# Optimization experiments

Hardware: AMD Instinct MI355X
Metric: run time of the kernel (lower is better)

Reference implementation:

```python
import jax, jax.numpy as jnp
import numpy as np

TEMPERATURE = 11.313708498984761  # sqrt(128)


def setup_inputs() -> dict:
    key = jax.random.key(0)
    kq, kk, kv = jax.random.split(key, 3)
    b, n, m, d, dv = 16, 2048, 2048, 128, 128
    return {
        "queries": jax.random.normal(kq, (b, n, d), dtype=jnp.float32),
        "keys": jax.random.normal(kk, (b, m, d), dtype=jnp.float32),
        "values": jax.random.normal(kv, (b, m, dv), dtype=jnp.float32),
    }


def reference(queries, keys, values):
    # scores: [b, n, m]
    scores = jnp.einsum('bnd,bmd->bnm', queries, keys) / TEMPERATURE
    attn = jax.nn.softmax(scores, axis=2)
    # out: [b, n, d']
    return jnp.einsum('bnm,bmd->bnd', attn, values)
```

## Files before the change

### kernel.cpp

```cpp
#include <hip/hip_runtime.h>


#define BATCH 16
#define SEQ   2048
#define DIM   128
#define NT    (SEQ / 64)

typedef short bf16x8 __attribute__((ext_vector_type(8)));
typedef float f32x16 __attribute__((ext_vector_type(16)));

static __device__ __forceinline__ unsigned pk2(float lo, float hi) {
  union { float f; unsigned u; } a, b;
  a.f = lo; b.f = hi;
  return ((b.u + 0x8000u) & 0xffff0000u) | ((a.u + 0x8000u) >> 16);
}
static __device__ __forceinline__ float fast_exp2(float x) {
#if __has_builtin(__builtin_amdgcn_exp2f)
  return __builtin_amdgcn_exp2f(x);
#else
  return exp2f(x);
#endif
}

typedef __attribute__((address_space(1))) const unsigned int g_u32;
typedef __attribute__((address_space(3))) unsigned int l_u32;
static __device__ __forceinline__ void gl2lds16(const unsigned short* g, unsigned short* l) {
  __builtin_amdgcn_global_load_lds((g_u32*)g, (l_u32*)l, 16, 0, 0);
}

__global__ __launch_bounds__(256)
void prep_kernel(const float* __restrict__ K, const float* __restrict__ V,
                 unsigned short* __restrict__ Kb, unsigned short* __restrict__ Vt,
                 float scale) {
  const int bx = blockIdx.x, tid = threadIdx.x;
  if (bx < 2048) {
    size_t idx = (size_t)bx * 256 + tid;
    const float4* kf = (const float4*)K;
    float4 a = kf[idx * 2], c = kf[idx * 2 + 1];
    uint4 o;
    o.x = pk2(a.x * scale, a.y * scale);
    o.y = pk2(a.z * scale, a.w * scale);
    o.z = pk2(c.x * scale, c.y * scale);
    o.w = pk2(c.z * scale, c.w * scale);
    ((uint4*)Kb)[idx] = o;
  } else {
    __shared__ float tile[128][33];
    const int vb = bx - 2048;
    const int b = vb >> 6, r = vb & 63;
    const int m0 = (r & 15) * 128, d0 = (r >> 4) * 32;
    const int c = tid & 7, mr = tid >> 3;
    const float* src = V + ((size_t)(b * SEQ) + m0) * DIM + d0;
#pragma unroll
    for (int it = 0; it < 4; ++it) {
      int m = it * 32 + mr;
      float4 x = *(const float4*)(src + (size_t)m * DIM + c * 4);
      tile[m][c * 4 + 0] = x.x; tile[m][c * 4 + 1] = x.y;
      tile[m][c * 4 + 2] = x.z; tile[m][c * 4 + 3] = x.w;
    }
    __syncthreads();
    const int dr = tid >> 3, s = tid & 7;
    unsigned short* dst = Vt + ((size_t)(b * DIM) + d0 + dr) * SEQ + m0;
#pragma unroll
    for (int it = 0; it < 2; ++it) {
      int slot = it * 8 + s;
      uint4 o;
      o.x = pk2(tile[slot * 8 + 0][dr], tile[slot * 8 + 1][dr]);
      o.y = pk2(tile[slot * 8 + 2][dr], tile[slot * 8 + 3][dr]);
      o.z = pk2(tile[slot * 8 + 4][dr], tile[slot * 8 + 5][dr]);
      o.w = pk2(tile[slot * 8 + 6][dr], tile[slot * 8 + 7][dr]);
      *(uint4*)(dst + slot * 8) = o;
    }
  }
}


__global__ __launch_bounds__(256, 2)
void attn_kernel(const float* __restrict__ Qf,
                 const unsigned short* __restrict__ Kb,
                 const unsigned short* __restrict__ Vtb,
                 float* __restrict__ out) {
  __shared__ __align__(1024) unsigned char smem[65536];
  unsigned short* sm16 = (unsigned short*)smem;

  const int tid  = threadIdx.x;
  const int wv   = tid >> 6;
  const int w_q  = wv & 1;
  const int w_m  = wv >> 1;
  const int lane = tid & 63;
  const int l31  = lane & 31;
  const int q2   = lane >> 5;
  const int b    = blockIdx.x;
  const int q0   = blockIdx.y * 64 + w_q * 32;

  const unsigned short* kb = Kb  + (size_t)b * SEQ * DIM;
  const unsigned short* vb = Vtb + (size_t)b * SEQ * DIM;

  bf16x8 aq[8];
  {
    const float* qp = Qf + ((size_t)(b * SEQ) + q0 + l31) * DIM + q2 * 8;
#pragma unroll
    for (int c = 0; c < 8; ++c) {
      float4 x = *(const float4*)(qp + c * 16);
      float4 y = *(const float4*)(qp + c * 16 + 4);
      union { unsigned i[4]; bf16x8 v; } u;
      u.i[0] = pk2(x.x, x.y); u.i[1] = pk2(x.z, x.w);
      u.i[2] = pk2(y.x, y.y); u.i[3] = pk2(y.z, y.w);
      aq[c] = u.v;
    }
  }

  unsigned kgo[4], vgo[4];
#pragma unroll
  for (int i = 0; i < 4; ++i) {
    int ch = wv * 4 + i;
    int krow = ch * 4 + (lane >> 4);
    kgo[i] = (unsigned)(krow * 128) + ((((lane & 15) << 4) ^ ((krow & 15) << 4)) >> 1);
    int vrow = ch * 8 + (lane >> 3);
    vgo[i] = (unsigned)(vrow * 2048) + ((((lane & 7) << 4) ^ ((vrow & 7) << 4)) >> 1);
  }

  const int kro = ((w_m * 32 + l31) << 8) + ((q2 << 4) ^ ((l31 & 15) << 4));
  const int vro = (l31 << 7) + (((w_m << 6) + (q2 << 4)) ^ ((l31 & 7) << 4));

  f32x16 oacc[4];
#pragma unroll
  for (int t = 0; t < 4; ++t)
#pragma unroll
    for (int i = 0; i < 16; ++i) oacc[t][i] = 0.0f;
  float lsum = 0.0f;

#define STAGE(TK, BUF) do {                                                  \
    const unsigned short* kt_b = kb + ((size_t)(TK) << 13);                  \
    const unsigned short* vt_b = vb + ((TK) << 6);                           \
    unsigned short* kd = sm16 + (((BUF) + wv * 4096) >> 1);                  \
    unsigned short* vd = sm16 + ((32768 + (BUF) + wv * 4096) >> 1);          \
    _Pragma("unroll")                                                        \
    for (int i = 0; i < 4; ++i) gl2lds16(kt_b + kgo[i], kd + i * 512);       \
    _Pragma("unroll")                                                        \
    for (int i = 0; i < 4; ++i) gl2lds16(vt_b + vgo[i], vd + i * 512);       \
  } while (0)

  STAGE(0, 0);

  for (int kt = 0; kt < NT; ++kt) {
    const int cur = (kt & 1) << 14;
    __syncthreads();
    if (kt + 1 < NT) STAGE(kt + 1, 16384 - cur);

    const unsigned char* kB = smem + cur;
    const unsigned char* vB = smem + 32768 + cur;

    f32x16 s;
#pragma unroll
    for (int i = 0; i < 16; ++i) s[i] = 0.0f;
    __builtin_amdgcn_s_setprio(1);
#pragma unroll
    for (int c = 0; c < 8; ++c) {
      bf16x8 bk = *(const bf16x8*)(kB + (kro ^ (c << 5)));
      s = __builtin_amdgcn_mfma_f32_32x32x16_bf16(bk, aq[c], s, 0, 0, 0);
    }
    __builtin_amdgcn_s_setprio(0);

    float p[16];
#pragma unroll
    for (int i = 0; i < 16; ++i) { p[i] = fast_exp2(s[i]); lsum += p[i]; }

    unsigned d0 = pk2(p[0], p[1]),   d1 = pk2(p[2], p[3]);
    unsigned d2 = pk2(p[4], p[5]),   d3 = pk2(p[6], p[7]);
    unsigned d4 = pk2(p[8], p[9]),   d5 = pk2(p[10], p[11]);
    unsigned d6 = pk2(p[12], p[13]), d7 = pk2(p[14], p[15]);
    asm("v_permlane32_swap_b32 %0, %1" : "+v"(d0), "+v"(d2));
    asm("v_permlane32_swap_b32 %0, %1" : "+v"(d1), "+v"(d3));
    asm("v_permlane32_swap_b32 %0, %1" : "+v"(d4), "+v"(d6));
    asm("v_permlane32_swap_b32 %0, %1" : "+v"(d5), "+v"(d7));
    union { unsigned u[4]; bf16x8 v; } pu0, pu1;
    pu0.u[0] = d0; pu0.u[1] = d1; pu0.u[2] = d2; pu0.u[3] = d3;
    pu1.u[0] = d4; pu1.u[1] = d5; pu1.u[2] = d6; pu1.u[3] = d7;

    __builtin_amdgcn_s_setprio(1);
#pragma unroll
    for (int t = 0; t < 4; ++t) {
      bf16x8 bv0 = *(const bf16x8*)(vB + t * 4096 + vro);
      oacc[t] = __builtin_amdgcn_mfma_f32_32x32x16_bf16(pu0.v, bv0, oacc[t], 0, 0, 0);
      bf16x8 bv1 = *(const bf16x8*)(vB + t * 4096 + (vro ^ 32));
      oacc[t] = __builtin_amdgcn_mfma_f32_32x32x16_bf16(pu1.v, bv1, oacc[t], 0, 0, 0);
    }
    __builtin_amdgcn_s_setprio(0);
  }
#undef STAGE

  lsum += __shfl_xor(lsum, 32, 64);

  __syncthreads();
  float* cb  = (float*)smem;
  float* cbL = (float*)(smem + 32768);
  if (w_m == 1) {
    float* my = cb + w_q * 4096;
#pragma unroll
    for (int t = 0; t < 4; ++t)
#pragma unroll
      for (int r = 0; r < 16; ++r)
        my[(t * 16 + r) * 64 + lane] = oacc[t][r];
  }
  cbL[w_m * 64 + w_q * 32 + l31] = lsum;
  __syncthreads();
  if (w_m == 0) {
    const float* pr = cb + w_q * 4096;
    float linv[16];
#pragma unroll
    for (int r = 0; r < 16; ++r) {
      int qr = (r & 3) + ((r >> 2) << 3) + (q2 << 2);
      linv[r] = 1.0f / (cbL[w_q * 32 + qr] + cbL[64 + w_q * 32 + qr]);
    }
    float* ob = out + ((size_t)(b * SEQ) + q0) * DIM;
#pragma unroll
    for (int t = 0; t < 4; ++t)
#pragma unroll
      for (int r = 0; r < 16; ++r) {
        int qr = (r & 3) + ((r >> 2) << 3) + (q2 << 2);
        ob[(size_t)qr * DIM + t * 32 + l31] = (oacc[t][r] + pr[(t * 16 + r) * 64 + lane]) * linv[r];
      }
  }
}

extern "C" void kernel_launch(void* const* d_in, const int* in_sizes, int n_in,
                              void* d_out, int out_size, void* d_ws, size_t ws_size,
                              hipStream_t stream) {
  const float* Q = (const float*)d_in[0];
  const float* K = (const float*)d_in[1];
  const float* V = (const float*)d_in[2];
  float* out = (float*)d_out;

  const size_t elems = (size_t)BATCH * SEQ * DIM;
  unsigned short* Kb = (unsigned short*)d_ws;
  unsigned short* Vt = Kb + elems;

  const double TEMPERATURE = 11.313708498984761;
  const float scale = (float)(1.4426950408889634 / TEMPERATURE);

  prep_kernel<<<3072, 256, 0, stream>>>(K, V, Kb, Vt, scale);
  attn_kernel<<<dim3(BATCH, SEQ / 64), 256, 0, stream>>>(Q, Kb, Vt, out);
}
```

Measured before the change: 136.5 us.

## Software-pipeline QK of next tile with softmax and PV of current tile

Restructures the attention loop into a two-stage software pipeline, so the QK^T MFMAs for tile k+1 are issued before the exp/convert/PV work for tile k. V fragments are preloaded into registers before the barrier, letting the stage buffer be reused earlier. The QK chain is split into two independent accumulators, row sums use four partial accumulators, and the manual bf16 rounding is replaced by the hardware v_cvt_pk_bf16_f32 instruction. This shortens dependency chains and overlaps the matrix units with the vector units, at the cost of higher register pressure and possible occupancy loss.

```diff
diff --git a/kernel.cpp b/kernel.cpp
--- a/kernel.cpp
+++ b/kernel.cpp
@@ -127,7 +127,7 @@
   for (int t = 0; t < 4; ++t)
 #pragma unroll
     for (int i = 0; i < 16; ++i) oacc[t][i] = 0.0f;
-  float lsum = 0.0f;
+  float ls[4] = {0.0f, 0.0f, 0.0f, 0.0f};
 
 #define STAGE(TK, BUF) do {                                                  \
     const unsigned short* kt_b = kb + ((size_t)(TK) << 13);                  \
@@ -140,55 +140,120 @@
     for (int i = 0; i < 4; ++i) gl2lds16(vt_b + vgo[i], vd + i * 512);       \
   } while (0)
 
+#define VLOAD(CUR) do {                                                      \
+    const unsigned char* vB_ = smem + 32768 + (CUR);                         \
+    _Pragma("unroll")                                                        \
+    for (int t = 0; t < 4; ++t) {                                            \
+      vr[2 * t]     = *(const bf16x8*)(vB_ + t * 4096 + vro);                \
+      vr[2 * t + 1] = *(const bf16x8*)(vB_ + t * 4096 + (vro ^ 32));         \
+    }                                                                        \
+  } while (0)
+
+#define QK(CUR, SD) do {                                                     \
+    const unsigned char* kB_ = smem + (CUR);                                 \
+    f32x16 se, so;                                                           \
+    _Pragma("unroll")                                                        \
+    for (int i = 0; i < 16; ++i) { se[i] = 0.0f; so[i] = 0.0f; }             \
+    __builtin_amdgcn_s_setprio(1);                                           \
+    _Pragma("unroll")                                                        \
+    for (int c = 0; c < 4; ++c) {                                            \
+      bf16x8 b0 = *(const bf16x8*)(kB_ + (kro ^ ((2 * c) << 5)));            \
+      se = __builtin_amdgcn_mfma_f32_32x32x16_bf16(b0, aq[2 * c], se, 0, 0, 0); \
+      bf16x8 b1 = *(const bf16x8*)(kB_ + (kro ^ ((2 * c + 1) << 5)));        \
+      so = __builtin_amdgcn_mfma_f32_32x32x16_bf16(b1, aq[2 * c + 1], so, 0, 0, 0); \
+    }                                                                        \
+    __builtin_amdgcn_s_setprio(0);                                           \
+    _Pragma("unroll")                                                        \
+    for (int i = 0; i < 16; ++i) SD[i] = se[i] + so[i];                      \
+  } while (0)
+
+#define SOFTMAX(S, PU0, PU1) do {                                            \
+    float p[16];                                                             \
+    _Pragma("unroll")                                                        \
+    for (int i = 0; i < 16; ++i) p[i] = fast_exp2(S[i]);                     \
+    _Pragma("unroll")                                                        \
+    for (int i = 0; i < 4; ++i) {                                            \
+      ls[0] += p[4 * i + 0]; ls[1] += p[4 * i + 1];                          \
+      ls[2] += p[4 * i + 2]; ls[3] += p[4 * i + 3];                          \
+    }                                                                        \
+    unsigned d0, d1, d2, d3, d4, d5, d6, d7;                                 \
+    asm("v_cvt_pk_bf16_f32 %0, %1, %2" : "=v"(d0) : "v"(p[0]),  "v"(p[1]));  \
+    asm("v_cvt_pk_bf16_f32 %0, %1, %2" : "=v"(d1) : "v"(p[2]),  "v"(p[3]));  \
+    asm("v_cvt_pk_bf16_f32 %0, %1, %2" : "=v"(d2) : "v"(p[4]),  "v"(p[5]));  \
+    asm("v_cvt_pk_bf16_f32 %0, %1, %2" : "=v"(d3) : "v"(p[6]),  "v"(p[7]));  \
+    asm("v_cvt_pk_bf16_f32 %0, %1, %2" : "=v"(d4) : "v"(p[8]),  "v"(p[9]));  \
+    asm("v_cvt_pk_bf16_f32 %0, %1, %2" : "=v"(d5) : "v"(p[10]), "v"(p[11])); \
+    asm("v_cvt_pk_bf16_f32 %0, %1, %2" : "=v"(d6) : "v"(p[12]), "v"(p[13])); \
+    asm("v_cvt_pk_bf16_f32 %0, %1, %2" : "=v"(d7) : "v"(p[14]), "v"(p[15])); \
+    asm("v_permlane32_swap_b32 %0, %1" : "+v"(d0), "+v"(d2));                \
+    asm("v_permlane32_swap_b32 %0, %1" : "+v"(d1), "+v"(d3));                \
+    asm("v_permlane32_swap_b32 %0, %1" : "+v"(d4), "+v"(d6));                \
+    asm("v_permlane32_swap_b32 %0, %1" : "+v"(d5), "+v"(d7));                \
+    PU0.u[0] = d0; PU0.u[1] = d1; PU0.u[2] = d2; PU0.u[3] = d3;              \
+    PU1.u[0] = d4; PU1.u[1] = d5; PU1.u[2] = d6; PU1.u[3] = d7;              \
+  } while (0)
+
+#define PV(PU0, PU1) do {                                                    \
+    __builtin_amdgcn_s_setprio(1);                                           \
+    _Pragma("unroll")                                                        \
+    for (int t = 0; t < 4; ++t) {                                            \
+      oacc[t] = __builtin_amdgcn_mfma_f32_32x32x16_bf16(PU0.v, vr[2 * t], oacc[t], 0, 0, 0); \
+      oacc[t] = __builtin_amdgcn_mfma_f32_32x32x16_bf16(PU1.v, vr[2 * t + 1], oacc[t], 0, 0, 0); \
+    }                                                                        \
+    __builtin_amdgcn_s_setprio(0);                                           \
+  } while (0)
+
+  bf16x8 vr[8];
+  f32x16 sA, sB;
+
   STAGE(0, 0);
-
-  for (int kt = 0; kt < NT; ++kt) {
-    const int cur = (kt & 1) << 14;
+  __syncthreads();
+  STAGE(1, 16384);
+  QK(0, sA);
+
+#pragma unroll 1
+  for (int t = 0; t < NT - 2; t += 2) {
+    {
+      VLOAD(0);
+      __syncthreads();
+      STAGE(t + 2, 0);
+      QK(16384, sB);
+      union { unsigned u[4]; bf16x8 v; } pu0, pu1;
+      SOFTMAX(sA, pu0, pu1);
+      PV(pu0, pu1);
+    }
+    {
+      VLOAD(16384);
+      __syncthreads();
+      STAGE(t + 3, 16384);
+      QK(0, sA);
+      union { unsigned u[4]; bf16x8 v; } pu0, pu1;
+      SOFTMAX(sB, pu0, pu1);
+      PV(pu0, pu1);
+    }
+  }
+  {
+    VLOAD(0);
     __syncthreads();
-    if (kt + 1 < NT) STAGE(kt + 1, 16384 - cur);
-
-    const unsigned char* kB = smem + cur;
-    const unsigned char* vB = smem + 32768 + cur;
-
-    f32x16 s;
-#pragma unroll
-    for (int i = 0; i < 16; ++i) s[i] = 0.0f;
-    __builtin_amdgcn_s_setprio(1);
-#pragma unroll
-    for (int c = 0; c < 8; ++c) {
-      bf16x8 bk = *(const bf16x8*)(kB + (kro ^ (c << 5)));
-      s = __builtin_amdgcn_mfma_f32_32x32x16_bf16(bk, aq[c], s, 0, 0, 0);
-    }
-    __builtin_amdgcn_s_setprio(0);
-
-    float p[16];
-#pragma unroll
-    for (int i = 0; i < 16; ++i) { p[i] = fast_exp2(s[i]); lsum += p[i]; }
-
-    unsigned d0 = pk2(p[0], p[1]),   d1 = pk2(p[2], p[3]);
-    unsigned d2 = pk2(p[4], p[5]),   d3 = pk2(p[6], p[7]);
-    unsigned d4 = pk2(p[8], p[9]),   d5 = pk2(p[10], p[11]);
-    unsigned d6 = pk2(p[12], p[13]), d7 = pk2(p[14], p[15]);
-    asm("v_permlane32_swap_b32 %0, %1" : "+v"(d0), "+v"(d2));
-    asm("v_permlane32_swap_b32 %0, %1" : "+v"(d1), "+v"(d3));
-    asm("v_permlane32_swap_b32 %0, %1" : "+v"(d4), "+v"(d6));
-    asm("v_permlane32_swap_b32 %0, %1" : "+v"(d5), "+v"(d7));
+    QK(16384, sB);
     union { unsigned u[4]; bf16x8 v; } pu0, pu1;
-    pu0.u[0] = d0; pu0.u[1] = d1; pu0.u[2] = d2; pu0.u[3] = d3;
-    pu1.u[0] = d4; pu1.u[1] = d5; pu1.u[2] = d6; pu1.u[3] = d7;
-
-    __builtin_amdgcn_s_setprio(1);
-#pragma unroll
-    for (int t = 0; t < 4; ++t) {
-      bf16x8 bv0 = *(const bf16x8*)(vB + t * 4096 + vro);
-      oacc[t] = __builtin_amdgcn_mfma_f32_32x32x16_bf16(pu0.v, bv0, oacc[t], 0, 0, 0);
-      bf16x8 bv1 = *(const bf16x8*)(vB + t * 4096 + (vro ^ 32));
-      oacc[t] = __builtin_amdgcn_mfma_f32_32x32x16_bf16(pu1.v, bv1, oacc[t], 0, 0, 0);
-    }
-    __builtin_amdgcn_s_setprio(0);
-  }
+    SOFTMAX(sA, pu0, pu1);
+    PV(pu0, pu1);
+  }
+  {
+    VLOAD(16384);
+    union { unsigned u[4]; bf16x8 v; } pu0, pu1;
+    SOFTMAX(sB, pu0, pu1);
+    PV(pu0, pu1);
+  }
+
 #undef STAGE
-
+#undef VLOAD
+#undef QK
+#undef SOFTMAX
+#undef PV
+
+  float lsum = (ls[0] + ls[1]) + (ls[2] + ls[3]);
   lsum += __shfl_xor(lsum, 32, 64);
 
   __syncthreads();
```

Result: no change. 137.8 us (+1.0%).
